# Kernel tuning notes

Measured on AMD Instinct MI355X. Metric: run time of the kernel, lower is better.

The kernel has to match this reference:

```python
import jax, jax.numpy as jnp
import numpy as np

N_USER = 100000
N_POI = 50000
D = 128
E = 1000000


def setup_inputs() -> dict:
    key = jax.random.key(0)
    ks = jax.random.split(key, 10)
    s = 1.0 / np.sqrt(D)  # glorot-ish scale for square weights
    return {
        "x_user": jax.random.normal(ks[0], (N_USER, D), jnp.float32),
        "x_poi": jax.random.normal(ks[1], (N_POI, D), jnp.float32),
        "W_u2p_src": jax.random.normal(ks[2], (D, D), jnp.float32) * s,
        "W_u2p_tgt": jax.random.normal(ks[3], (D, D), jnp.float32) * s,
        "W_p2u_src": jax.random.normal(ks[4], (D, D), jnp.float32) * s,
        "W_p2u_tgt": jax.random.normal(ks[5], (D, D), jnp.float32) * s,
        "e_u2p_src": jax.random.randint(ks[6], (E,), 0, N_USER, jnp.int32),
        "e_u2p_tgt": jax.random.randint(ks[7], (E,), 0, N_POI, jnp.int32),
        "e_p2u_src": jax.random.randint(ks[8], (E,), 0, N_POI, jnp.int32),
        "e_p2u_tgt": jax.random.randint(ks[9], (E,), 0, N_USER, jnp.int32),
    }


def _segment_mean(msgs, idx, num_segments):
    # scatter(..., reduce='mean') into a zero-initialized out:
    # targets with no incoming edges stay exactly zero.
    sums = jax.ops.segment_sum(msgs, idx, num_segments=num_segments)
    cnt = jax.ops.segment_sum(jnp.ones((idx.shape[0], 1), msgs.dtype), idx,
                              num_segments=num_segments)
    return sums / jnp.maximum(cnt, 1.0)


def reference(x_user, x_poi, W_u2p_src, W_u2p_tgt, W_p2u_src, W_p2u_tgt,
              e_u2p_src, e_u2p_tgt, e_p2u_src, e_p2u_tgt):
    # edge type user -> poi
    src = x_user @ W_u2p_src            # [N_USER, D]
    tgt = x_poi @ W_u2p_tgt             # [N_POI, D]
    msgs = src[e_u2p_src]               # gather [E, D]
    out_poi = tgt + _segment_mean(msgs, e_u2p_tgt, N_POI)

    # edge type poi -> user (reverse)
    src2 = x_poi @ W_p2u_src            # [N_POI, D]
    tgt2 = x_user @ W_p2u_tgt           # [N_USER, D]
    msgs2 = src2[e_p2u_src]             # gather [E, D]
    out_user = tgt2 + _segment_mean(msgs2, e_p2u_tgt, N_USER)

    # div = 1 per target type (one edge type per target); then relu
    out_user = jax.nn.relu(out_user)
    out_poi = jax.nn.relu(out_poi)
    # stack the hetero output dict as a single array [N_USER+N_POI, D]
    return jnp.concatenate([out_user, out_poi], axis=0)
```

## Files before the change

kernel.cpp:

```cpp
#include <hip/hip_runtime.h>
#include <hip/hip_bf16.h>

#define D 128
#define CHUNK 4096
#define BINSZ 128

typedef __attribute__((ext_vector_type(8))) short bf16x8;
typedef __attribute__((ext_vector_type(4))) float f32x4;

__device__ __forceinline__ ushort f2bf(float f) {
    uint u = __float_as_uint(f);
    u += 0x7fffu + ((u >> 16) & 1u);
    return (ushort)(u >> 16);
}

__device__ __forceinline__ int wave_incl_scan(int v) {
    int lane = threadIdx.x & 63;
#pragma unroll
    for (int off = 1; off < 64; off <<= 1) {
        int n = __shfl_up(v, off, 64);
        if (lane >= off) v += n;
    }
    return v;
}

__global__ __launch_bounds__(256) void cast_k(
        const float* __restrict__ xu, ushort* __restrict__ xbu, long long n4u,
        const float* __restrict__ xp, ushort* __restrict__ xbp, long long n4p) {
    long long g = (long long)blockIdx.x * 256 + threadIdx.x;
    long long gs = (long long)gridDim.x * 256;
    for (long long i = g; i < n4u; i += gs) {
        float4 v = ((const float4*)xu)[i];
        ushort4 o = {f2bf(v.x), f2bf(v.y), f2bf(v.z), f2bf(v.w)};
        ((ushort4*)xbu)[i] = o;
    }
    for (long long i = g; i < n4p; i += gs) {
        float4 v = ((const float4*)xp)[i];
        ushort4 o = {f2bf(v.x), f2bf(v.y), f2bf(v.z), f2bf(v.w)};
        ((ushort4*)xbp)[i] = o;
    }
}

__global__ __launch_bounds__(256) void hist_k(
        const int* __restrict__ etU, int EU, int* __restrict__ cntU, int NBu, int CBu,
        const int* __restrict__ etP, int EP, int* __restrict__ cntP, int NBp, int CBp) {
    __shared__ int h[800];
    const int* et; int E; int* cnt; int NB, CB, c;
    if (blockIdx.x < (unsigned)CBu) { et = etU; E = EU; cnt = cntU; NB = NBu; CB = CBu; c = blockIdx.x; }
    else { et = etP; E = EP; cnt = cntP; NB = NBp; CB = CBp; c = blockIdx.x - CBu; }
    for (int i = threadIdx.x; i < NB; i += 256) h[i] = 0;
    __syncthreads();
    int lo = c * CHUNK, hi = min(lo + CHUNK, E);
    for (int i = lo + threadIdx.x; i < hi; i += 256) atomicAdd(&h[et[i] >> 7], 1);
    __syncthreads();
    for (int i = threadIdx.x; i < NB; i += 256) cnt[(long long)i * CB + c] = h[i];
}

__global__ __launch_bounds__(256) void binscan_k(
        int* __restrict__ cntU, int* __restrict__ totU, int NBu, int CBu,
        int* __restrict__ cntP, int* __restrict__ totP, int NBp, int CBp) {
    int gw = (blockIdx.x * 256 + threadIdx.x) >> 6;
    int lane = threadIdx.x & 63;
    int* cnt; int* tot; int CB, bin;
    if (gw < NBu) { cnt = cntU; tot = totU; CB = CBu; bin = gw; }
    else {
        bin = gw - NBu;
        if (bin >= NBp) return;
        cnt = cntP; tot = totP; CB = CBp;
    }
    int* row = cnt + (long long)bin * CB;
    int carry = 0;
    for (int r = 0; r * 64 < CB; r++) {
        int i = r * 64 + lane;
        int v = (i < CB) ? row[i] : 0;
        int isc = wave_incl_scan(v);
        if (i < CB) row[i] = isc - v + carry;
        carry += __shfl(isc, 63, 64);
    }
    if (lane == 0) tot[bin] = carry;
}

__global__ __launch_bounds__(256) void mid_k(
        const int* __restrict__ totU, int* __restrict__ bstU, int NBu,
        const int* __restrict__ totP, int* __restrict__ bstP, int NBp,
        const float* __restrict__ W0, const float* __restrict__ W1,
        const float* __restrict__ W2, const float* __restrict__ W3,
        ushort* __restrict__ P) {
    if (blockIdx.x == 0) {
        if (threadIdx.x < 128) {
            int lane = threadIdx.x & 63;
            int w = threadIdx.x >> 6;
            const int* tot = w ? totP : totU;
            int* bst = w ? bstP : bstU;
            int nb = w ? NBp : NBu;
            int carry = 0;
            for (int r = 0; r * 64 < nb; r++) {
                int i = r * 64 + lane;
                int v = (i < nb) ? tot[i] : 0;
                int isc = wave_incl_scan(v);
                if (i < nb) bst[i] = isc - v + carry;
                carry += __shfl(isc, 63, 64);
            }
        }
        return;
    }
    int t = (blockIdx.x - 1) * 256 + threadIdx.x;
    if (t >= 4 * 2048) return;
    int w = t >> 11, r = t & 2047;
    int lane = r & 63, fi = r >> 6;
    int kk = fi >> 3, n0 = fi & 7;
    const float* W = (w == 0) ? W0 : (w == 1) ? W1 : (w == 2) ? W2 : W3;
    int col = n0 * 16 + (lane & 15);
    int kb = kk * 32 + (lane >> 4) * 8;
    bf16x8 v;
#pragma unroll
    for (int j = 0; j < 8; j++) v[j] = (short)f2bf(W[(kb + j) * D + col]);
    *(bf16x8*)&P[(long long)t * 8] = v;
}

__global__ __launch_bounds__(256) void binsort_k(
        const int* __restrict__ esU, const int* __restrict__ etU, int EU,
        const int* __restrict__ cntU, const int* __restrict__ bstU,
        int* __restrict__ binU, int NBu, int CBu,
        const int* __restrict__ esP, const int* __restrict__ etP, int EP,
        const int* __restrict__ cntP, const int* __restrict__ bstP,
        int* __restrict__ binP, int NBp, int CBp) {
    __shared__ int cur[800];
    const int* es; const int* et; int E; const int* cnt; const int* bst;
    int* bnd; int NB, CB, c;
    if (blockIdx.x < (unsigned)CBu) {
        es = esU; et = etU; E = EU; cnt = cntU; bst = bstU; bnd = binU;
        NB = NBu; CB = CBu; c = blockIdx.x;
    } else {
        es = esP; et = etP; E = EP; cnt = cntP; bst = bstP; bnd = binP;
        NB = NBp; CB = CBp; c = blockIdx.x - CBu;
    }
    for (int i = threadIdx.x; i < NB; i += 256)
        cur[i] = bst[i] + cnt[(long long)i * CB + c];
    __syncthreads();
    int lo = c * CHUNK, hi = min(lo + CHUNK, E);
    for (int i = lo + threadIdx.x; i < hi; i += 256) {
        int t = et[i];
        int s = es[i];
        int pos = atomicAdd(&cur[t >> 7], 1);
        bnd[pos] = ((t & 127) << 17) | s;
    }
}

__global__ __launch_bounds__(256) void csr_k(
        const int* __restrict__ binU, const int* __restrict__ bstU,
        const int* __restrict__ totU, int NBu,
        int* __restrict__ degU, int* __restrict__ startU, int* __restrict__ permU, int n_u,
        const int* __restrict__ binP, const int* __restrict__ bstP,
        const int* __restrict__ totP, int NBp,
        int* __restrict__ degP, int* __restrict__ startP, int* __restrict__ permP, int n_p) {
    __shared__ int h[128];
    __shared__ int base[128];
    __shared__ int cur[128];
    const int* bnd; const int* bst; const int* tot;
    int* deg; int* start; int* perm; int n, bin;
    if (blockIdx.x < (unsigned)NBu) {
        bnd = binU; bst = bstU; tot = totU; deg = degU; start = startU; perm = permU;
        n = n_u; bin = blockIdx.x;
    } else {
        bin = blockIdx.x - NBu;
        bnd = binP; bst = bstP; tot = totP; deg = degP; start = startP; perm = permP;
        n = n_p;
    }
    const int tid = threadIdx.x;
    int s0 = bst[bin], cnt = tot[bin];
    if (tid < 128) h[tid] = 0;
    __syncthreads();
    for (int i = s0 + tid; i < s0 + cnt; i += 256) atomicAdd(&h[bnd[i] >> 17], 1);
    __syncthreads();
    if (tid < 64) {
        int carry = 0;
#pragma unroll
        for (int r = 0; r < 2; r++) {
            int i = r * 64 + tid;
            int v = h[i];
            int isc = wave_incl_scan(v);
            base[i] = isc - v + carry;
            carry += __shfl(isc, 63, 64);
        }
    }
    __syncthreads();
    int t0 = bin << 7;
    if (tid < 128) {
        int t = t0 + tid;
        if (t < n) { deg[t] = h[tid]; start[t] = s0 + base[tid]; }
        cur[tid] = s0 + base[tid];
    }
    __syncthreads();
    for (int i = s0 + tid; i < s0 + cnt; i += 256) {
        int v = bnd[i];
        int pos = atomicAdd(&cur[v >> 17], 1);
        perm[pos] = v & 0x1FFFF;
    }
}

__global__ __launch_bounds__(256) void gather_k(
        const ushort* __restrict__ xb_poi, const int* __restrict__ perm_u,
        const int* __restrict__ start_u, const int* __restrict__ deg_u,
        uint* __restrict__ out_u, int n_user,
        const ushort* __restrict__ xb_user, const int* __restrict__ perm_p,
        const int* __restrict__ start_p, const int* __restrict__ deg_p,
        uint* __restrict__ out_p, int n_poi) {
    int gw = (blockIdx.x * 256 + threadIdx.x) >> 6;
    int lane = threadIdx.x & 63;
    const ushort* xb; const int* perm; const int* start; const int* deg; uint* out; int t;
    if (gw < n_user) { xb = xb_poi; perm = perm_u; start = start_u; deg = deg_u; out = out_u; t = gw; }
    else {
        t = gw - n_user;
        if (t >= n_poi) return;
        xb = xb_user; perm = perm_p; start = start_p; deg = deg_p; out = out_p;
    }
    const uint* x2 = (const uint*)xb;
    int s0 = start[t], dg = deg[t];
    float ax = 0.f, ay = 0.f;
    int j = 0;
    for (; j + 4 <= dg; j += 4) {
        int sa = perm[s0 + j], sb = perm[s0 + j + 1];
        int sc = perm[s0 + j + 2], sd = perm[s0 + j + 3];
        uint va = x2[sa * 64 + lane], vb = x2[sb * 64 + lane];
        uint vc = x2[sc * 64 + lane], vd = x2[sd * 64 + lane];
        ax += (__uint_as_float(va << 16) + __uint_as_float(vb << 16)) +
              (__uint_as_float(vc << 16) + __uint_as_float(vd << 16));
        ay += (__uint_as_float(va & 0xffff0000u) + __uint_as_float(vb & 0xffff0000u)) +
              (__uint_as_float(vc & 0xffff0000u) + __uint_as_float(vd & 0xffff0000u));
    }
    for (; j < dg; j++) {
        int s = perm[s0 + j];
        uint v = x2[s * 64 + lane];
        ax += __uint_as_float(v << 16);
        ay += __uint_as_float(v & 0xffff0000u);
    }
    float scl = 1.0f / fmaxf((float)dg, 1.0f);
    uint o = ((uint)f2bf(ay * scl) << 16) | (uint)f2bf(ax * scl);
    out[(long long)t * 128 + lane] = o;
}

__global__ __launch_bounds__(256) void mfma_k(
        const ushort* __restrict__ Xb_u, const ushort* __restrict__ WtP_u,
        const ushort* __restrict__ WsP_u, float* __restrict__ OUT_u, int n_u, int bu,
        const ushort* __restrict__ Xb_p, const ushort* __restrict__ WtP_p,
        const ushort* __restrict__ WsP_p, float* __restrict__ OUT_p, int n_p) {
    const ushort* Xb; const ushort* WtP; const ushort* WsP; float* OUT; int nrows, bbase;
    if (blockIdx.x < (unsigned)bu) { Xb = Xb_u; WtP = WtP_u; WsP = WsP_u; OUT = OUT_u; nrows = n_u; bbase = blockIdx.x; }
    else { Xb = Xb_p; WtP = WtP_p; WsP = WsP_p; OUT = OUT_p; nrows = n_p; bbase = blockIdx.x - bu; }
    const ushort* Agg = (const ushort*)OUT;

    const int tid = threadIdx.x;
    const int lane = tid & 63;
    const int wv = tid >> 6;
    const int waveRow = bbase * 128 + wv * 32;
    const int l15 = lane & 15, lhi = lane >> 4;

    f32x4 acc[2][8];
#pragma unroll
    for (int m = 0; m < 2; m++)
#pragma unroll
        for (int n = 0; n < 8; n++) acc[m][n] = (f32x4){0.f, 0.f, 0.f, 0.f};

#pragma unroll
    for (int p = 0; p < 2; p++) {
        const ushort* Wp = p ? WsP : WtP;
#pragma unroll
        for (int kk = 0; kk < 4; kk++) {
            bf16x8 a[2];
#pragma unroll
            for (int m = 0; m < 2; m++) {
                int r = waveRow + m * 16 + l15;
                if (r > nrows - 1) r = nrows - 1;
                a[m] = p ? *(const bf16x8*)&Agg[(long long)r * 256 + kk * 32 + lhi * 8]
                         : *(const bf16x8*)&Xb[(long long)r * D + kk * 32 + lhi * 8];
            }
#pragma unroll
            for (int n = 0; n < 8; n++) {
                bf16x8 b = *(const bf16x8*)&Wp[(long long)((kk * 8 + n) * 64 + lane) * 8];
#pragma unroll
                for (int m = 0; m < 2; m++)
                    acc[m][n] = __builtin_amdgcn_mfma_f32_16x16x32_bf16(a[m], b, acc[m][n], 0, 0, 0);
            }
        }
    }

#pragma unroll
    for (int m = 0; m < 2; m++)
#pragma unroll
        for (int n = 0; n < 8; n++)
#pragma unroll
            for (int ri = 0; ri < 4; ri++) {
                int r = waveRow + m * 16 + lhi * 4 + ri;
                if (r < nrows)
                    OUT[(long long)r * D + n * 16 + l15] = fmaxf(acc[m][n][ri], 0.f);
            }
}

extern "C" void kernel_launch(void* const* d_in, const int* in_sizes, int n_in,
                              void* d_out, int out_size, void* d_ws, size_t ws_size,
                              hipStream_t stream) {
    const float* x_user    = (const float*)d_in[0];
    const float* x_poi     = (const float*)d_in[1];
    const float* W_u2p_src = (const float*)d_in[2];
    const float* W_u2p_tgt = (const float*)d_in[3];
    const float* W_p2u_src = (const float*)d_in[4];
    const float* W_p2u_tgt = (const float*)d_in[5];
    const int* e_u2p_src   = (const int*)d_in[6];
    const int* e_u2p_tgt   = (const int*)d_in[7];
    const int* e_p2u_src   = (const int*)d_in[8];
    const int* e_p2u_tgt   = (const int*)d_in[9];

    const int n_user = in_sizes[0] / D;
    const int n_poi  = in_sizes[1] / D;
    const int E1 = in_sizes[6];
    const int E2 = in_sizes[8];

    float* out = (float*)d_out;
    float* out_user = out;
    float* out_poi  = out + (long long)n_user * D;

    const int NBu = (n_user + BINSZ - 1) / BINSZ;
    const int NBp = (n_poi + BINSZ - 1) / BINSZ;
    const int CBu = (E2 + CHUNK - 1) / CHUNK;
    const int CBp = (E1 + CHUNK - 1) / CHUNK;

    char* w = (char*)d_ws;
    ushort* xb_user = (ushort*)w;  w += (size_t)n_user * D * 2;
    ushort* xb_poi  = (ushort*)w;  w += (size_t)n_poi  * D * 2;
    ushort* Wpack   = (ushort*)w;  w += (size_t)4 * 2048 * 8 * 2;
    int* binU       = (int*)w;     w += (size_t)E2 * 4;
    int* binP       = (int*)w;     w += (size_t)E1 * 4;
    int* perm_user  = (int*)w;     w += (size_t)E2 * 4;
    int* perm_poi   = (int*)w;     w += (size_t)E1 * 4;
    int* cntU       = (int*)w;     w += (size_t)NBu * CBu * 4;
    int* cntP       = (int*)w;     w += (size_t)NBp * CBp * 4;
    int* totU       = (int*)w;     w += (size_t)NBu * 4;
    int* totP       = (int*)w;     w += (size_t)NBp * 4;
    int* bstU       = (int*)w;     w += (size_t)NBu * 4;
    int* bstP       = (int*)w;     w += (size_t)NBp * 4;
    int* deg_user   = (int*)w;     w += (size_t)n_user * 4;
    int* deg_poi    = (int*)w;     w += (size_t)n_poi * 4;
    int* start_user = (int*)w;     w += (size_t)n_user * 4;
    int* start_poi  = (int*)w;     w += (size_t)n_poi * 4;

    ushort* WtP_user = Wpack + 0 * 2048 * 8;
    ushort* WsP_user = Wpack + 1 * 2048 * 8;
    ushort* WtP_poi  = Wpack + 2 * 2048 * 8;
    ushort* WsP_poi  = Wpack + 3 * 2048 * 8;

    cast_k<<<2048, 256, 0, stream>>>(x_user, xb_user, (long long)n_user * D / 4,
                                     x_poi, xb_poi, (long long)n_poi * D / 4);

    hist_k<<<CBu + CBp, 256, 0, stream>>>(e_p2u_tgt, E2, cntU, NBu, CBu,
                                          e_u2p_tgt, E1, cntP, NBp, CBp);

    {
        int nw = NBu + NBp;
        binscan_k<<<(nw + 3) / 4, 256, 0, stream>>>(cntU, totU, NBu, CBu,
                                                    cntP, totP, NBp, CBp);
    }

    mid_k<<<33, 256, 0, stream>>>(totU, bstU, NBu, totP, bstP, NBp,
                                  W_p2u_tgt, W_p2u_src, W_u2p_tgt, W_u2p_src, Wpack);

    binsort_k<<<CBu + CBp, 256, 0, stream>>>(
        e_p2u_src, e_p2u_tgt, E2, cntU, bstU, binU, NBu, CBu,
        e_u2p_src, e_u2p_tgt, E1, cntP, bstP, binP, NBp, CBp);

    csr_k<<<NBu + NBp, 256, 0, stream>>>(
        binU, bstU, totU, NBu, deg_user, start_user, perm_user, n_user,
        binP, bstP, totP, NBp, deg_poi, start_poi, perm_poi, n_poi);

    gather_k<<<(n_user + n_poi + 3) / 4, 256, 0, stream>>>(
        xb_poi, perm_user, start_user, deg_user, (uint*)out_user, n_user,
        xb_user, perm_poi, start_poi, deg_poi, (uint*)out_poi, n_poi);

    int bu = (n_user + 127) / 128, bp = (n_poi + 127) / 128;
    mfma_k<<<bu + bp, 256, 0, stream>>>(xb_user, WtP_user, WsP_user, out_user, n_user, bu,
                                        xb_poi, WtP_poi, WsP_poi, out_poi, n_poi);
}
```

Baseline: 360.3 us.

## Fuse CSR build, neighbor gather-mean, and MFMA GEMM into one per-bin kernel

Replaces the separate csr_k, gather_k and mfma_k launches with one kernel per 128-target bin. Each bin's edge sources are sorted into LDS, with a global spill buffer for overflow. The mean-aggregated rows are staged in LDS as bf16 and fed straight into the MFMA projection alongside the target transform. This removes the global perm/deg/start arrays, the intermediate bf16 aggregate written into the output buffer, and two launches. In exchange the block is larger, uses heavy LDS (about 50KB), which lowers occupancy, and serialises the gather per wave over 16 targets.

```diff
diff --git a/kernel.cpp b/kernel.cpp
--- a/kernel.cpp
+++ b/kernel.cpp
@@ -4,6 +4,7 @@
 #define D 128
 #define CHUNK 4096
 #define BINSZ 128
+#define CAP 4096
 
 typedef __attribute__((ext_vector_type(8))) short bf16x8;
 typedef __attribute__((ext_vector_type(4))) float f32x4;
@@ -147,31 +148,43 @@
     }
 }
 
-__global__ __launch_bounds__(256) void csr_k(
-        const int* __restrict__ binU, const int* __restrict__ bstU,
-        const int* __restrict__ totU, int NBu,
-        int* __restrict__ degU, int* __restrict__ startU, int* __restrict__ permU, int n_u,
-        const int* __restrict__ binP, const int* __restrict__ bstP,
-        const int* __restrict__ totP, int NBp,
-        int* __restrict__ degP, int* __restrict__ startP, int* __restrict__ permP, int n_p) {
-    __shared__ int h[128];
-    __shared__ int base[128];
-    __shared__ int cur[128];
-    const int* bnd; const int* bst; const int* tot;
-    int* deg; int* start; int* perm; int n, bin;
+__global__ __launch_bounds__(512) void fused_k(
+        const int* __restrict__ bndU, const int* __restrict__ bstU,
+        const int* __restrict__ totU, int NBu, int* __restrict__ spillU,
+        const ushort* __restrict__ gsrcU, const ushort* __restrict__ XbU,
+        const ushort* __restrict__ WtPU, const ushort* __restrict__ WsPU,
+        float* __restrict__ OUTU, int n_u,
+        const int* __restrict__ bndP, const int* __restrict__ bstP,
+        const int* __restrict__ totP, int* __restrict__ spillP,
+        const ushort* __restrict__ gsrcP, const ushort* __restrict__ XbP,
+        const ushort* __restrict__ WtPP, const ushort* __restrict__ WsPP,
+        float* __restrict__ OUTP, int n_p) {
+    __shared__ int eLds[CAP];
+    __shared__ ushort agg[128][136];
+    __shared__ int h[128], sbase[128], scur[128];
+
+    const int* bnd; const int* bst; const int* tot; int* spill;
+    const ushort* gsrc; const ushort* Xb; const ushort* WtP; const ushort* WsP;
+    float* OUT; int n, bb;
     if (blockIdx.x < (unsigned)NBu) {
-        bnd = binU; bst = bstU; tot = totU; deg = degU; start = startU; perm = permU;
-        n = n_u; bin = blockIdx.x;
+        bnd = bndU; bst = bstU; tot = totU; spill = spillU; gsrc = gsrcU; Xb = XbU;
+        WtP = WtPU; WsP = WsPU; OUT = OUTU; n = n_u; bb = blockIdx.x;
     } else {
-        bin = blockIdx.x - NBu;
-        bnd = binP; bst = bstP; tot = totP; deg = degP; start = startP; perm = permP;
-        n = n_p;
+        bb = blockIdx.x - NBu;
+        bnd = bndP; bst = bstP; tot = totP; spill = spillP; gsrc = gsrcP; Xb = XbP;
+        WtP = WtPP; WsP = WsPP; OUT = OUTP; n = n_p;
     }
     const int tid = threadIdx.x;
-    int s0 = bst[bin], cnt = tot[bin];
+    const int lane = tid & 63;
+    const int wv = tid >> 6;
+    const int t0 = bb << 7;
+    const int s0 = bst[bb];
+    const int cnt = tot[bb];
+
     if (tid < 128) h[tid] = 0;
     __syncthreads();
-    for (int i = s0 + tid; i < s0 + cnt; i += 256) atomicAdd(&h[bnd[i] >> 17], 1);
+    for (int i = s0 + tid; i < s0 + cnt; i += 512)
+        atomicAdd(&h[bnd[i] >> 17], 1);
     __syncthreads();
     if (tid < 64) {
         int carry = 0;
@@ -180,121 +193,90 @@
             int i = r * 64 + tid;
             int v = h[i];
             int isc = wave_incl_scan(v);
-            base[i] = isc - v + carry;
+            sbase[i] = isc - v + carry;
             carry += __shfl(isc, 63, 64);
         }
     }
     __syncthreads();
-    int t0 = bin << 7;
-    if (tid < 128) {
-        int t = t0 + tid;
-        if (t < n) { deg[t] = h[tid]; start[t] = s0 + base[tid]; }
-        cur[tid] = s0 + base[tid];
-    }
-    __syncthreads();
-    for (int i = s0 + tid; i < s0 + cnt; i += 256) {
+    if (tid < 128) scur[tid] = sbase[tid];
+    __syncthreads();
+    for (int i = s0 + tid; i < s0 + cnt; i += 512) {
         int v = bnd[i];
-        int pos = atomicAdd(&cur[v >> 17], 1);
-        perm[pos] = v & 0x1FFFF;
-    }
-}
-
-__global__ __launch_bounds__(256) void gather_k(
-        const ushort* __restrict__ xb_poi, const int* __restrict__ perm_u,
-        const int* __restrict__ start_u, const int* __restrict__ deg_u,
-        uint* __restrict__ out_u, int n_user,
-        const ushort* __restrict__ xb_user, const int* __restrict__ perm_p,
-        const int* __restrict__ start_p, const int* __restrict__ deg_p,
-        uint* __restrict__ out_p, int n_poi) {
-    int gw = (blockIdx.x * 256 + threadIdx.x) >> 6;
-    int lane = threadIdx.x & 63;
-    const ushort* xb; const int* perm; const int* start; const int* deg; uint* out; int t;
-    if (gw < n_user) { xb = xb_poi; perm = perm_u; start = start_u; deg = deg_u; out = out_u; t = gw; }
-    else {
-        t = gw - n_user;
-        if (t >= n_poi) return;
-        xb = xb_user; perm = perm_p; start = start_p; deg = deg_p; out = out_p;
-    }
-    const uint* x2 = (const uint*)xb;
-    int s0 = start[t], dg = deg[t];
-    float ax = 0.f, ay = 0.f;
-    int j = 0;
-    for (; j + 4 <= dg; j += 4) {
-        int sa = perm[s0 + j], sb = perm[s0 + j + 1];
-        int sc = perm[s0 + j + 2], sd = perm[s0 + j + 3];
-        uint va = x2[sa * 64 + lane], vb = x2[sb * 64 + lane];
-        uint vc = x2[sc * 64 + lane], vd = x2[sd * 64 + lane];
-        ax += (__uint_as_float(va << 16) + __uint_as_float(vb << 16)) +
-              (__uint_as_float(vc << 16) + __uint_as_float(vd << 16));
-        ay += (__uint_as_float(va & 0xffff0000u) + __uint_as_float(vb & 0xffff0000u)) +
-              (__uint_as_float(vc & 0xffff0000u) + __uint_as_float(vd & 0xffff0000u));
-    }
-    for (; j < dg; j++) {
-        int s = perm[s0 + j];
-        uint v = x2[s * 64 + lane];
-        ax += __uint_as_float(v << 16);
-        ay += __uint_as_float(v & 0xffff0000u);
-    }
-    float scl = 1.0f / fmaxf((float)dg, 1.0f);
-    uint o = ((uint)f2bf(ay * scl) << 16) | (uint)f2bf(ax * scl);
-    out[(long long)t * 128 + lane] = o;
-}
-
-__global__ __launch_bounds__(256) void mfma_k(
-        const ushort* __restrict__ Xb_u, const ushort* __restrict__ WtP_u,
-        const ushort* __restrict__ WsP_u, float* __restrict__ OUT_u, int n_u, int bu,
-        const ushort* __restrict__ Xb_p, const ushort* __restrict__ WtP_p,
-        const ushort* __restrict__ WsP_p, float* __restrict__ OUT_p, int n_p) {
-    const ushort* Xb; const ushort* WtP; const ushort* WsP; float* OUT; int nrows, bbase;
-    if (blockIdx.x < (unsigned)bu) { Xb = Xb_u; WtP = WtP_u; WsP = WsP_u; OUT = OUT_u; nrows = n_u; bbase = blockIdx.x; }
-    else { Xb = Xb_p; WtP = WtP_p; WsP = WsP_p; OUT = OUT_p; nrows = n_p; bbase = blockIdx.x - bu; }
-    const ushort* Agg = (const ushort*)OUT;
-
-    const int tid = threadIdx.x;
-    const int lane = tid & 63;
-    const int wv = tid >> 6;
-    const int waveRow = bbase * 128 + wv * 32;
+        int pos = atomicAdd(&scur[v >> 17], 1);
+        int src = v & 0x1FFFF;
+        if (pos < CAP) eLds[pos] = src;
+        else spill[s0 + pos] = src;
+    }
+    __syncthreads();
+
+    const uint* x2 = (const uint*)gsrc;
+#pragma unroll 1
+    for (int q = 0; q < 16; q++) {
+        int lt = wv * 16 + q;
+        int b0 = sbase[lt], dg = h[lt];
+        float ax = 0.f, ay = 0.f;
+        int j = 0;
+        for (; j + 4 <= dg; j += 4) {
+            int p = b0 + j;
+            int sa = (p     < CAP) ? eLds[p]     : spill[s0 + p];
+            int sb = (p + 1 < CAP) ? eLds[p + 1] : spill[s0 + p + 1];
+            int sc = (p + 2 < CAP) ? eLds[p + 2] : spill[s0 + p + 2];
+            int sd = (p + 3 < CAP) ? eLds[p + 3] : spill[s0 + p + 3];
+            uint va = x2[sa * 64 + lane], vb = x2[sb * 64 + lane];
+            uint vc = x2[sc * 64 + lane], vd = x2[sd * 64 + lane];
+            ax += (__uint_as_float(va << 16) + __uint_as_float(vb << 16)) +
+                  (__uint_as_float(vc << 16) + __uint_as_float(vd << 16));
+            ay += (__uint_as_float(va & 0xffff0000u) + __uint_as_float(vb & 0xffff0000u)) +
+                  (__uint_as_float(vc & 0xffff0000u) + __uint_as_float(vd & 0xffff0000u));
+        }
+        for (; j < dg; j++) {
+            int p = b0 + j;
+            int s = (p < CAP) ? eLds[p] : spill[s0 + p];
+            uint v = x2[s * 64 + lane];
+            ax += __uint_as_float(v << 16);
+            ay += __uint_as_float(v & 0xffff0000u);
+        }
+        float scl = 1.0f / fmaxf((float)dg, 1.0f);
+        uint o = ((uint)f2bf(ay * scl) << 16) | (uint)f2bf(ax * scl);
+        *(uint*)&agg[lt][2 * lane] = o;
+    }
+    __syncthreads();
+
     const int l15 = lane & 15, lhi = lane >> 4;
-
-    f32x4 acc[2][8];
-#pragma unroll
-    for (int m = 0; m < 2; m++)
-#pragma unroll
-        for (int n = 0; n < 8; n++) acc[m][n] = (f32x4){0.f, 0.f, 0.f, 0.f};
-
-#pragma unroll
-    for (int p = 0; p < 2; p++) {
-        const ushort* Wp = p ? WsP : WtP;
-#pragma unroll
-        for (int kk = 0; kk < 4; kk++) {
-            bf16x8 a[2];
-#pragma unroll
-            for (int m = 0; m < 2; m++) {
-                int r = waveRow + m * 16 + l15;
-                if (r > nrows - 1) r = nrows - 1;
-                a[m] = p ? *(const bf16x8*)&Agg[(long long)r * 256 + kk * 32 + lhi * 8]
-                         : *(const bf16x8*)&Xb[(long long)r * D + kk * 32 + lhi * 8];
-            }
-#pragma unroll
-            for (int n = 0; n < 8; n++) {
-                bf16x8 b = *(const bf16x8*)&Wp[(long long)((kk * 8 + n) * 64 + lane) * 8];
-#pragma unroll
-                for (int m = 0; m < 2; m++)
-                    acc[m][n] = __builtin_amdgcn_mfma_f32_16x16x32_bf16(a[m], b, acc[m][n], 0, 0, 0);
-            }
-        }
-    }
-
-#pragma unroll
-    for (int m = 0; m < 2; m++)
-#pragma unroll
-        for (int n = 0; n < 8; n++)
-#pragma unroll
-            for (int ri = 0; ri < 4; ri++) {
-                int r = waveRow + m * 16 + lhi * 4 + ri;
-                if (r < nrows)
-                    OUT[(long long)r * D + n * 16 + l15] = fmaxf(acc[m][n][ri], 0.f);
-            }
+    f32x4 acc[8];
+#pragma unroll
+    for (int nn = 0; nn < 8; nn++) acc[nn] = (f32x4){0.f, 0.f, 0.f, 0.f};
+
+    int rA = t0 + wv * 16 + l15;
+    if (rA > n - 1) rA = n - 1;
+#pragma unroll
+    for (int kk = 0; kk < 4; kk++) {
+        bf16x8 a0 = *(const bf16x8*)&Xb[(long long)rA * D + kk * 32 + lhi * 8];
+#pragma unroll
+        for (int nn = 0; nn < 8; nn++) {
+            bf16x8 b = *(const bf16x8*)&WtP[(long long)((kk * 8 + nn) * 64 + lane) * 8];
+            acc[nn] = __builtin_amdgcn_mfma_f32_16x16x32_bf16(a0, b, acc[nn], 0, 0, 0);
+        }
+    }
+    const int rl = wv * 16 + l15;
+#pragma unroll
+    for (int kk = 0; kk < 4; kk++) {
+        bf16x8 a1 = *(const bf16x8*)&agg[rl][kk * 32 + lhi * 8];
+#pragma unroll
+        for (int nn = 0; nn < 8; nn++) {
+            bf16x8 b = *(const bf16x8*)&WsP[(long long)((kk * 8 + nn) * 64 + lane) * 8];
+            acc[nn] = __builtin_amdgcn_mfma_f32_16x16x32_bf16(a1, b, acc[nn], 0, 0, 0);
+        }
+    }
+
+#pragma unroll
+    for (int nn = 0; nn < 8; nn++)
+#pragma unroll
+        for (int ri = 0; ri < 4; ri++) {
+            int r = t0 + wv * 16 + lhi * 4 + ri;
+            if (r < n)
+                OUT[(long long)r * D + nn * 16 + l15] = fmaxf(acc[nn][ri], 0.f);
+        }
 }
 
 extern "C" void kernel_launch(void* const* d_in, const int* in_sizes, int n_in,
@@ -331,18 +313,14 @@
     ushort* Wpack   = (ushort*)w;  w += (size_t)4 * 2048 * 8 * 2;
     int* binU       = (int*)w;     w += (size_t)E2 * 4;
     int* binP       = (int*)w;     w += (size_t)E1 * 4;
-    int* perm_user  = (int*)w;     w += (size_t)E2 * 4;
-    int* perm_poi   = (int*)w;     w += (size_t)E1 * 4;
+    int* spillU     = (int*)w;     w += (size_t)E2 * 4;
+    int* spillP     = (int*)w;     w += (size_t)E1 * 4;
     int* cntU       = (int*)w;     w += (size_t)NBu * CBu * 4;
     int* cntP       = (int*)w;     w += (size_t)NBp * CBp * 4;
     int* totU       = (int*)w;     w += (size_t)NBu * 4;
     int* totP       = (int*)w;     w += (size_t)NBp * 4;
     int* bstU       = (int*)w;     w += (size_t)NBu * 4;
     int* bstP       = (int*)w;     w += (size_t)NBp * 4;
-    int* deg_user   = (int*)w;     w += (size_t)n_user * 4;
-    int* deg_poi    = (int*)w;     w += (size_t)n_poi * 4;
-    int* start_user = (int*)w;     w += (size_t)n_user * 4;
-    int* start_poi  = (int*)w;     w += (size_t)n_poi * 4;
 
     ushort* WtP_user = Wpack + 0 * 2048 * 8;
     ushort* WsP_user = Wpack + 1 * 2048 * 8;
@@ -355,11 +333,8 @@
     hist_k<<<CBu + CBp, 256, 0, stream>>>(e_p2u_tgt, E2, cntU, NBu, CBu,
                                           e_u2p_tgt, E1, cntP, NBp, CBp);
 
-    {
-        int nw = NBu + NBp;
-        binscan_k<<<(nw + 3) / 4, 256, 0, stream>>>(cntU, totU, NBu, CBu,
-                                                    cntP, totP, NBp, CBp);
-    }
+    binscan_k<<<(NBu + NBp + 3) / 4, 256, 0, stream>>>(cntU, totU, NBu, CBu,
+                                                       cntP, totP, NBp, CBp);
 
     mid_k<<<33, 256, 0, stream>>>(totU, bstU, NBu, totP, bstP, NBp,
                                   W_p2u_tgt, W_p2u_src, W_u2p_tgt, W_u2p_src, Wpack);
@@ -368,15 +343,9 @@
         e_p2u_src, e_p2u_tgt, E2, cntU, bstU, binU, NBu, CBu,
         e_u2p_src, e_u2p_tgt, E1, cntP, bstP, binP, NBp, CBp);
 
-    csr_k<<<NBu + NBp, 256, 0, stream>>>(
-        binU, bstU, totU, NBu, deg_user, start_user, perm_user, n_user,
-        binP, bstP, totP, NBp, deg_poi, start_poi, perm_poi, n_poi);
-
-    gather_k<<<(n_user + n_poi + 3) / 4, 256, 0, stream>>>(
-        xb_poi, perm_user, start_user, deg_user, (uint*)out_user, n_user,
-        xb_user, perm_poi, start_poi, deg_poi, (uint*)out_poi, n_poi);
-
-    int bu = (n_user + 127) / 128, bp = (n_poi + 127) / 128;
-    mfma_k<<<bu + bp, 256, 0, stream>>>(xb_user, WtP_user, WsP_user, out_user, n_user, bu,
-                                        xb_poi, WtP_poi, WsP_poi, out_poi, n_poi);
-}
+    fused_k<<<NBu + NBp, 512, 0, stream>>>(
+        binU, bstU, totU, NBu, spillU, xb_poi, xb_user,
+        WtP_user, WsP_user, out_user, n_user,
+        binP, bstP, totP, spillP, xb_user, xb_poi,
+        WtP_poi, WsP_poi, out_poi, n_poi);
+}
```

After: 339.2 us. 1.06x faster.
